# Kernel tuning notes

Hardware: AMD Instinct MI355X
Metric: run time of the kernel (lower is better)

The kernel has to match this reference:

```python
import jax, jax.numpy as jnp
import numpy as np
from jax.scipy.special import logsumexp

B, S, H, T = 64, 512, 768, 9

def setup_inputs() -> dict:
    key = jax.random.key(0)
    ks = jax.random.split(key, 6)
    return {
        "encoder_out": jax.random.normal(ks[0], (B, S, H), jnp.float32),
        "labels": jax.random.randint(ks[1], (B, S), 0, T, jnp.int32),
        "mask": jnp.ones((B, S), jnp.int32),
        "lengths": jnp.full((B,), S, jnp.int32),
        "fc_w": jax.random.normal(ks[2], (T, H), jnp.float32) * 0.02,
        "fc_b": jnp.zeros((T,), jnp.float32),
        "start_trans": jax.random.uniform(ks[3], (T,), jnp.float32, -0.1, 0.1),
        "end_trans": jax.random.uniform(ks[4], (T,), jnp.float32, -0.1, 0.1),
        "trans": jax.random.uniform(ks[5], (T, T), jnp.float32, -0.1, 0.1),
    }

def crf_log_likelihood(em, tg, mk, start, end, trans):
    # em: [S,B,T], tg: [S,B], mk: [S,B] float. torchcrf forward (reduction='none').
    barange = jnp.arange(em.shape[1])
    # --- numerator: score of the gold path ---
    score0 = start[tg[0]] + em[0][barange, tg[0]]
    def num_step(carry, x):
        score, prev = carry
        em_i, tg_i, mk_i = x
        score = score + (trans[prev, tg_i] + em_i[barange, tg_i]) * mk_i
        prev = jnp.where(mk_i > 0, tg_i, prev)
        return (score, prev), None
    (score, prev), _ = jax.lax.scan(num_step, (score0, tg[0]), (em[1:], tg[1:], mk[1:]))
    numerator = score + end[prev]
    # --- denominator: log partition via forward algorithm ---
    alpha = start[None, :] + em[0]  # [B,T]
    def den_step(alpha, x):
        em_i, mk_i = x
        nxt = logsumexp(alpha[:, :, None] + trans[None] + em_i[:, None, :], axis=1)
        return jnp.where(mk_i[:, None] > 0, nxt, alpha), None
    alpha, _ = jax.lax.scan(den_step, alpha, (em[1:], mk[1:]))
    denominator = logsumexp(alpha + end[None, :], axis=1)
    return numerator - denominator  # [B]

def crf_viterbi(em, mk, start, end, trans):
    # em: [S,B,T], mk: [S,B] float. Returns best path [S,B].
    barange = jnp.arange(em.shape[1])
    alpha = start[None, :] + em[0]  # [B,T]
    idT = jnp.arange(em.shape[2])[None, :]
    def fwd_step(alpha, x):
        em_i, mk_i = x
        scores = alpha[:, :, None] + trans[None]  # [B, T_prev, T_cur]
        bp = jnp.argmax(scores, axis=1)           # [B,T]
        nxt = jnp.max(scores, axis=1) + em_i
        valid = mk_i[:, None] > 0
        return jnp.where(valid, nxt, alpha), jnp.where(valid, bp, idT)
    alpha, bps = jax.lax.scan(fwd_step, alpha, (em[1:], mk[1:]))  # bps: [S-1,B,T]
    last = jnp.argmax(alpha + end[None, :], axis=1)  # [B]
    def back_step(tag, bp):
        prev = bp[barange, tag]
        return prev, prev
    _, path_head = jax.lax.scan(back_step, last, bps, reverse=True)  # [S-1,B]
    return jnp.concatenate([path_head, last[None, :]], axis=0)  # [S,B]

def reference(encoder_out, labels, mask, lengths, fc_w, fc_b, start_trans, end_trans, trans):
    # dropout in eval mode == identity
    emissions = jnp.einsum('bsh,th->bst', encoder_out, fc_w) + fc_b  # [B,S,T]
    em = jnp.swapaxes(emissions, 0, 1)               # [S,B,T]
    tg = jnp.swapaxes(labels, 0, 1)                  # [S,B]
    mk = jnp.swapaxes(mask, 0, 1).astype(emissions.dtype)
    ll = crf_log_likelihood(em, tg, mk, start_trans, end_trans, trans)  # [B]
    ner_loss = jnp.mean(-ll)
    path = crf_viterbi(em, mk, start_trans, end_trans, trans)  # [S,B]
    ner_predict = jnp.swapaxes(path, 0, 1)  # [B,S]
    return ner_loss, ner_predict, lengths
```

## Files before the change

kernel.cpp:

```cpp
#include <hip/hip_runtime.h>

#define Bsz 64
#define Ssz 512
#define Hsz 768
#define Tsz 9
#define NCH 16
#define LOG2E 1.4426950408889634f
#define LN2F  0.6931471805599453f
#define PSTR 17

__device__ __forceinline__ int SK(int s) { return s * Tsz + ((s >> 5) << 1); }

__global__ __launch_bounds__(256, 1) void emis_kernel(
    const float* __restrict__ x, const float* __restrict__ fcw,
    const float* __restrict__ fcb, float* __restrict__ em,
    int* __restrict__ cnt) {
    __shared__ __align__(16) float4 w4[Tsz * Hsz / 4];
    __shared__ float bias[Tsz];
    __shared__ float part[16 * Tsz * PSTR];
    const int tid = threadIdx.x;
    if (blockIdx.x == 0 && tid == 0) *cnt = 0;
    const float4* fw4 = reinterpret_cast<const float4*>(fcw);
#pragma unroll
    for (int i = 0; i < 7; ++i) {
        const int o = tid + i * 256;
        if (o < 1728) w4[o] = fw4[o];
    }
    if (tid < Tsz) bias[tid] = fcb[tid];
    __syncthreads();

    const int p = tid >> 4, l = tid & 15;
    const size_t pos0 = (size_t)blockIdx.x * 32;
    const float4* xr0 = reinterpret_cast<const float4*>(x + (pos0 + p) * Hsz);
    const float4* xr1 = reinterpret_cast<const float4*>(x + (pos0 + 16 + p) * Hsz);

    float acc[Tsz][2];
#pragma unroll
    for (int t = 0; t < Tsz; ++t) { acc[t][0] = 0.0f; acc[t][1] = 0.0f; }

#pragma unroll 4
    for (int i = 0; i < 12; ++i) {
        const float4 xv0 = xr0[i * 16 + l];
        const float4 xv1 = xr1[i * 16 + l];
#pragma unroll
        for (int t = 0; t < Tsz; ++t) {
            const float4 wv = w4[t * 192 + i * 16 + l];
            acc[t][0] = fmaf(xv0.x, wv.x, fmaf(xv0.y, wv.y,
                        fmaf(xv0.z, wv.z, fmaf(xv0.w, wv.w, acc[t][0]))));
            acc[t][1] = fmaf(xv1.x, wv.x, fmaf(xv1.y, wv.y,
                        fmaf(xv1.z, wv.z, fmaf(xv1.w, wv.w, acc[t][1]))));
        }
    }

#pragma unroll
    for (int k = 0; k < 2; ++k) {
        __syncthreads();
#pragma unroll
        for (int t = 0; t < Tsz; ++t) part[(p * Tsz + t) * PSTR + l] = acc[t][k];
        __syncthreads();
        if (tid < 16 * Tsz) {
            const int pq = tid / Tsz, t = tid - pq * Tsz;
            float s = bias[t];
#pragma unroll
            for (int l2 = 0; l2 < 16; ++l2) s += part[(pq * Tsz + t) * PSTR + l2];
            em[(pos0 + (size_t)k * 16 + pq) * Tsz + t] = s;
        }
    }
}

__global__ __launch_bounds__(256, 1) void scan_kernel(
    const float* __restrict__ em, const int* __restrict__ mask,
    const float* __restrict__ trans, float* __restrict__ R2,
    float* __restrict__ MV) {
    __shared__ float Tlds[81];
    __shared__ float Elds[81];
    const int tid = threadIdx.x;
    if (tid < 81) {
        const float t = trans[tid];
        Tlds[tid] = t;
        Elds[tid] = exp2f(t * LOG2E);
    }
    __syncthreads();

    const int wid = tid >> 6, ln = tid & 63;
    const int q = ln / 9;
    const int j = ln - q * 9;
    const int W = blockIdx.x * 4 + wid;
    const int rho = W * 7 + q;
    if (q >= 7 || rho >= 2048 * Tsz) return;

    const int a = rho % Tsz;
    const int bc2 = rho / Tsz;
    const bool isLSE = bc2 < 1024;
    const int bc = isLSE ? bc2 : bc2 - 1024;
    const int b = bc >> 4, c = bc & 15;
    const int lb = 9 * q;

    const float* emb = em + (size_t)b * Ssz * Tsz;
    const int* mkb = mask + b * Ssz;
    const int s_lo = c * 32 + 1;
    const int s_hi = min(c * 32 + 32, Ssz - 1);

    float ec = emb[s_lo * Tsz + j];
    int mc = mkb[s_lo];

    if (isLSE) {
        float Ecol[Tsz];
#pragma unroll
        for (int i = 0; i < Tsz; ++i) Ecol[i] = Elds[i * Tsz + j];
        float pp = (j == a) ? 1.0f : 0.0f;
        float K = 0.0f;
        for (int s = s_lo; s <= s_hi; ++s) {
            const int sp = (s < s_hi) ? s + 1 : s;
            const float en = emb[sp * Tsz + j];
            const int mn = mkb[sp];
            float g = __shfl(pp, lb, 64) * Ecol[0];
#pragma unroll
            for (int i = 1; i < Tsz; ++i)
                g = fmaf(__shfl(pp, lb + i, 64), Ecol[i], g);
            const float np = g * exp2f(ec * LOG2E);
            if (mc > 0) pp = np;
            if (((s - s_lo) & 7) == 7) {
                float ss = __shfl(pp, lb, 64);
#pragma unroll
                for (int i = 1; i < Tsz; ++i) ss += __shfl(pp, lb + i, 64);
                K += __log2f(ss);
                const float inv = 1.0f / ss;
                pp *= inv;
            }
            ec = en; mc = mn;
        }
        R2[((size_t)bc * Tsz + a) * Tsz + j] = K + __log2f(pp);
    } else {
        float Tcol[Tsz];
#pragma unroll
        for (int i = 0; i < Tsz; ++i) Tcol[i] = Tlds[i * Tsz + j];
        float pp = (j == a) ? 0.0f : -1e30f;
        for (int s = s_lo; s <= s_hi; ++s) {
            const int sp = (s < s_hi) ? s + 1 : s;
            const float en = emb[sp * Tsz + j];
            const int mn = mkb[sp];
            float g = __shfl(pp, lb, 64) + Tcol[0];
#pragma unroll
            for (int i = 1; i < Tsz; ++i)
                g = fmaxf(g, __shfl(pp, lb + i, 64) + Tcol[i]);
            if (mc > 0) pp = g + ec;
            ec = en; mc = mn;
        }
        MV[(size_t)bc * 81 + a * Tsz + j] = pp;
    }
}

__device__ __forceinline__ void amax9(const float (&v)[Tsz], float& bv, int& bi) {
    float w01v = (v[1] > v[0]) ? v[1] : v[0]; int w01i = (v[1] > v[0]) ? 1 : 0;
    float w23v = (v[3] > v[2]) ? v[3] : v[2]; int w23i = (v[3] > v[2]) ? 3 : 2;
    float w45v = (v[5] > v[4]) ? v[5] : v[4]; int w45i = (v[5] > v[4]) ? 5 : 4;
    float w67v = (v[7] > v[6]) ? v[7] : v[6]; int w67i = (v[7] > v[6]) ? 7 : 6;
    float x03v = (w23v > w01v) ? w23v : w01v; int x03i = (w23v > w01v) ? w23i : w01i;
    float x47v = (w67v > w45v) ? w67v : w45v; int x47i = (w67v > w45v) ? w67i : w45i;
    float y07v = (x47v > x03v) ? x47v : x03v; int y07i = (x47v > x03v) ? x47i : x03i;
    bv = (v[8] > y07v) ? v[8] : y07v;
    bi = (v[8] > y07v) ? 8 : y07i;
}

__global__ __launch_bounds__(192, 1) void vit3_kernel(
    const float* __restrict__ em, const int* __restrict__ labels,
    const int* __restrict__ mask, const int* __restrict__ lengths,
    const float* __restrict__ start_t, const float* __restrict__ end_t,
    const float* __restrict__ trans, const float* __restrict__ R2,
    const float* __restrict__ MV, float* __restrict__ out_path,
    float* __restrict__ ll, float* __restrict__ dout, int* __restrict__ cnt) {
    __shared__ __align__(16) float em_s[4640];
    __shared__ __align__(16) int   mk_s[Ssz];
    __shared__ __align__(16) float mv_s[NCH * 81];
    __shared__ __align__(16) float r2_s[NCH * 81];
    __shared__ float tr_s[81];
    __shared__ float st_s[12], en_s[12];
    __shared__ __align__(16) float alc[2][NCH][12];
    __shared__ float a2c[2][12];
    __shared__ unsigned char bp[(Ssz - 1) * Tsz];
    __shared__ unsigned char mapA[64][12], mapB[64][12];
    __shared__ float den_sh, num_sh;
    __shared__ int lastf;

    const int b = blockIdx.x, tid = threadIdx.x;
    const int wv = tid >> 6, ln = tid & 63;
    const int c = tid / 12, j9 = tid % 12;
    const float* emb = em + (size_t)b * Ssz * Tsz;
    const int* mkb = mask + b * Ssz;
    const int* lbb = labels + b * Ssz;

    for (int i = tid; i < Ssz * Tsz; i += 192) {
        const int s = i / 9, j = i - s * 9;
        em_s[SK(s) + j] = emb[i];
    }
    for (int i = tid; i < Ssz; i += 192) mk_s[i] = mkb[i];
    {
        const float4* v4 = reinterpret_cast<const float4*>(MV + (size_t)b * NCH * 81);
        float4* vd = reinterpret_cast<float4*>(mv_s);
        for (int i = tid; i < NCH * 81 / 4; i += 192) vd[i] = v4[i];
        const float4* r4 = reinterpret_cast<const float4*>(R2 + (size_t)b * NCH * 81);
        float4* rd = reinterpret_cast<float4*>(r2_s);
        for (int i = tid; i < NCH * 81 / 4; i += 192) rd[i] = r4[i];
        if (tid < 81) tr_s[tid] = trans[tid];
        if (tid >= 96 && tid < 96 + Tsz) {
            st_s[tid - 96] = start_t[tid - 96];
            en_s[tid - 96] = end_t[tid - 96];
        }
    }
    __syncthreads();

    float tc[Tsz];
    const int jj = (j9 < Tsz) ? j9 : Tsz - 1;
#pragma unroll
    for (int i = 0; i < Tsz; ++i) tc[i] = tr_s[i * Tsz + jj];

    float aj = 0.0f;
    if (c == 0 && j9 < Tsz) {
        aj = st_s[j9] + em_s[j9];
        alc[0][0][j9] = aj;
    }
    if (wv == 1 && ln < Tsz) a2c[0][ln] = (st_s[ln] + em_s[ln]) * LOG2E;

    for (int r = 0; r < NCH; ++r) {
        __syncthreads();
        if (r < NCH - 1 && c == r + 1 && j9 < Tsz) {
            const float* M = &mv_s[r * 81];
            float m = alc[0][r][0] + M[j9];
#pragma unroll
            for (int i = 1; i < Tsz; ++i)
                m = fmaxf(m, alc[0][r][i] + M[i * Tsz + j9]);
            aj = m;
            alc[0][c][j9] = m;
        }
        if (wv == 1 && ln < Tsz) {
            const float* Rr = &r2_s[r * 81];
            float xi[Tsz];
#pragma unroll
            for (int i = 0; i < Tsz; ++i) xi[i] = a2c[r & 1][i] + Rr[i * Tsz + ln];
            float m = xi[0];
#pragma unroll
            for (int i = 1; i < Tsz; ++i) m = fmaxf(m, xi[i]);
            float sm = 0.0f;
#pragma unroll
            for (int i = 0; i < Tsz; ++i) sm += exp2f(xi[i] - m);
            a2c[(r + 1) & 1][ln] = m + __log2f(sm);
        }
    }

    int pb = 0;
    for (int k = 0; k < 32; ++k) {
        __syncthreads();
        const int s = c * 32 + 1 + k;
        if (j9 < Tsz && s <= Ssz - 1) {
            const int mk = mk_s[s];
            float av[12];
            const float4* ap = reinterpret_cast<const float4*>(&alc[pb][c][0]);
            *reinterpret_cast<float4*>(&av[0]) = ap[0];
            *reinterpret_cast<float4*>(&av[4]) = ap[1];
            *reinterpret_cast<float4*>(&av[8]) = ap[2];
            float v[Tsz];
#pragma unroll
            for (int i = 0; i < Tsz; ++i) v[i] = av[i] + tc[i];
            float bv; int bi;
            amax9(v, bv, bi);
            bp[(s - 1) * Tsz + j9] = (unsigned char)((mk > 0) ? bi : j9);
            if (mk > 0) aj = bv + em_s[SK(s) + j9];
        }
        if (j9 < Tsz) alc[1 - pb][c][j9] = aj;
        pb ^= 1;
    }
    __syncthreads();

    float bb = alc[0][NCH - 1][0] + en_s[0];
    int last = 0;
#pragma unroll
    for (int q = 1; q < Tsz; ++q) {
        const float qq = alc[0][NCH - 1][q] + en_s[q];
        if (qq > bb) { bb = qq; last = q; }
    }

    const int lo = ln * 8;
    const int hi = min(lo + 7, Ssz - 2);
    if (wv == 0) {
        int xf[Tsz];
#pragma unroll
        for (int t = 0; t < Tsz; ++t) xf[t] = t;
        for (int k = hi; k >= lo; --k) {
#pragma unroll
            for (int t = 0; t < Tsz; ++t) xf[t] = bp[k * Tsz + xf[t]];
        }
#pragma unroll
        for (int t = 0; t < Tsz; ++t) mapA[ln][t] = (unsigned char)xf[t];
    } else if (wv == 1) {
        if (ln == 0) {
            float xv[Tsz];
#pragma unroll
            for (int i = 0; i < Tsz; ++i) xv[i] = a2c[0][i] + en_s[i] * LOG2E;
            float m = xv[0];
#pragma unroll
            for (int i = 1; i < Tsz; ++i) m = fmaxf(m, xv[i]);
            float sm = 0.0f;
#pragma unroll
            for (int i = 0; i < Tsz; ++i) sm += exp2f(xv[i] - m);
            den_sh = m + __log2f(sm);
        }
    } else {
        float part = 0.0f;
        for (int s = 1 + ln; s < Ssz; s += 64) {
            if (mk_s[s] > 0) {
                const int tg = lbb[s];
                int pq = s - 1;
                while (pq > 0 && mk_s[pq] == 0) --pq;
                part += tr_s[lbb[pq] * Tsz + tg] + em_s[SK(s) + tg];
            }
        }
#pragma unroll
        for (int off = 32; off >= 1; off >>= 1) part += __shfl_xor(part, off, 64);
        if (ln == 0) {
            const int tg0 = lbb[0];
            float num = part + st_s[tg0] + em_s[tg0];
            int pq = Ssz - 1;
            while (pq > 0 && mk_s[pq] == 0) --pq;
            num += en_s[lbb[pq]];
            num_sh = num;
        }
    }

#define VIT_RND(CUR, NXT, D)                                               \
    {                                                                      \
        unsigned char nn[Tsz];                                             \
        if (wv == 0) {                                                     \
            const int o = ln + (D);                                        \
            if (o < 64) {                                                  \
                _Pragma("unroll") for (int t = 0; t < Tsz; ++t)            \
                    nn[t] = CUR[ln][CUR[o][t]];                            \
            } else {                                                       \
                _Pragma("unroll") for (int t = 0; t < Tsz; ++t)            \
                    nn[t] = CUR[ln][t];                                    \
            }                                                              \
        }                                                                  \
        __syncthreads();                                                   \
        if (wv == 0) {                                                     \
            _Pragma("unroll") for (int t = 0; t < Tsz; ++t)                \
                NXT[ln][t] = nn[t];                                        \
        }                                                                  \
        __syncthreads();                                                   \
    }
    VIT_RND(mapA, mapB, 1)
    VIT_RND(mapB, mapA, 2)
    VIT_RND(mapA, mapB, 4)
    VIT_RND(mapB, mapA, 8)
    VIT_RND(mapA, mapB, 16)
    VIT_RND(mapB, mapA, 32)
#undef VIT_RND

    if (wv == 0) {
        int t = (ln == 63) ? last : (int)mapA[ln + 1][last];
        float* op = out_path + (size_t)b * Ssz;
        for (int k = hi; k >= lo; --k) {
            t = bp[k * Tsz + t];
            op[k] = (float)t;
        }
        if (ln == 0) op[Ssz - 1] = (float)last;
    }
    if (b == 0 && wv == 2) dout[1 + Bsz * Ssz + ln] = (float)lengths[ln];

    if (tid == 0) {
        ll[b] = num_sh - den_sh * LN2F;
        __threadfence();
        lastf = (atomicAdd(cnt, 1) == Bsz - 1) ? 1 : 0;
    }
    __syncthreads();
    if (lastf && wv == 0) {
        __threadfence();
        float v = ll[ln];
#pragma unroll
        for (int off = 32; off >= 1; off >>= 1) v += __shfl_xor(v, off, 64);
        if (ln == 0) dout[0] = -v * (1.0f / (float)Bsz);
    }
}

extern "C" void kernel_launch(void* const* d_in, const int* in_sizes, int n_in,
                              void* d_out, int out_size, void* d_ws, size_t ws_size,
                              hipStream_t stream) {
    const float* enc    = (const float*)d_in[0];
    const int*   labels = (const int*)d_in[1];
    const int*   mask   = (const int*)d_in[2];
    const int*   lengths= (const int*)d_in[3];
    const float* fcw    = (const float*)d_in[4];
    const float* fcb    = (const float*)d_in[5];
    const float* startt = (const float*)d_in[6];
    const float* endt   = (const float*)d_in[7];
    const float* trans  = (const float*)d_in[8];

    float* out = (float*)d_out;
    float* em  = (float*)d_ws;
    float* R2  = em + (size_t)Bsz * Ssz * Tsz;
    float* MV  = R2 + (size_t)Bsz * NCH * 81;
    float* ll  = MV + (size_t)Bsz * NCH * 81;
    int*   cnt = (int*)(ll + Bsz);

    emis_kernel<<<Bsz * Ssz / 32, 256, 0, stream>>>(enc, fcw, fcb, em, cnt);
    const int row_tasks = 2 * Bsz * NCH * Tsz;
    scan_kernel<<<(row_tasks + 27) / 28, 256, 0, stream>>>(em, mask, trans, R2, MV);
    vit3_kernel<<<Bsz, 192, 0, stream>>>(em, labels, mask, lengths, startt, endt,
                                         trans, R2, MV, out + 1, ll, out, cnt);
}
```

Measured before the change: 65.87 us.

## Fuse emission projection with per-chunk CRF scan into a single kernel

Merges the emission GEMV kernel and the chunked forward/Viterbi scan kernel into one kernel, one block per 32-step chunk. Each block keeps its emissions and mask in shared memory and recomputes the first emission row of the next chunk, so the scan no longer reads em back from global memory and one launch is removed. The cost is some redundant projection work per block and only 18 of 256 threads running the serial scan, which leaves most of the block idle during that phase.

Measured after the change: 71.03 us. +7.8%, slower.

```diff
diff --git a/kernel.cpp b/kernel.cpp
--- a/kernel.cpp
+++ b/kernel.cpp
@@ -11,15 +11,27 @@
 
 __device__ __forceinline__ int SK(int s) { return s * Tsz + ((s >> 5) << 1); }
 
-__global__ __launch_bounds__(256, 1) void emis_kernel(
+__global__ __launch_bounds__(256, 1) void emscan2_kernel(
     const float* __restrict__ x, const float* __restrict__ fcw,
-    const float* __restrict__ fcb, float* __restrict__ em,
-    int* __restrict__ cnt) {
+    const float* __restrict__ fcb, const int* __restrict__ mask,
+    const float* __restrict__ trans, float* __restrict__ em,
+    float* __restrict__ R2, float* __restrict__ MV, int* __restrict__ cnt) {
     __shared__ __align__(16) float4 w4[Tsz * Hsz / 4];
     __shared__ float bias[Tsz];
     __shared__ float part[16 * Tsz * PSTR];
+    __shared__ float em_w[33 * Tsz];
+    __shared__ int   mk_w[33];
+    __shared__ float Elds[81];
+    __shared__ float Tlds[81];
+
     const int tid = threadIdx.x;
-    if (blockIdx.x == 0 && tid == 0) *cnt = 0;
+    const int bc = blockIdx.x;
+    const int b = bc >> 4, c = bc & 15;
+    const int base = c * 32;
+    const size_t pos0 = (size_t)bc * 32;
+
+    if (bc == 0 && tid == 0) *cnt = 0;
+
     const float4* fw4 = reinterpret_cast<const float4*>(fcw);
 #pragma unroll
     for (int i = 0; i < 7; ++i) {
@@ -27,100 +39,108 @@
         if (o < 1728) w4[o] = fw4[o];
     }
     if (tid < Tsz) bias[tid] = fcb[tid];
+    if (tid >= 16 && tid < 16 + 81) {
+        const float t = trans[tid - 16];
+        Tlds[tid - 16] = t;
+        Elds[tid - 16] = exp2f(t * LOG2E);
+    }
+    if (tid >= 128 && tid < 128 + 33) {
+        const int s = base + (tid - 128);
+        mk_w[tid - 128] = (s < Ssz) ? mask[b * Ssz + s] : 0;
+    }
     __syncthreads();
 
     const int p = tid >> 4, l = tid & 15;
-    const size_t pos0 = (size_t)blockIdx.x * 32;
-    const float4* xr0 = reinterpret_cast<const float4*>(x + (pos0 + p) * Hsz);
-    const float4* xr1 = reinterpret_cast<const float4*>(x + (pos0 + 16 + p) * Hsz);
-
-    float acc[Tsz][2];
-#pragma unroll
-    for (int t = 0; t < Tsz; ++t) { acc[t][0] = 0.0f; acc[t][1] = 0.0f; }
-
+    {
+        const float4* xr0 = reinterpret_cast<const float4*>(x + (pos0 + p) * Hsz);
+        const float4* xr1 = reinterpret_cast<const float4*>(x + (pos0 + 16 + p) * Hsz);
+        float acc[Tsz][2];
+#pragma unroll
+        for (int t = 0; t < Tsz; ++t) { acc[t][0] = 0.0f; acc[t][1] = 0.0f; }
 #pragma unroll 4
-    for (int i = 0; i < 12; ++i) {
-        const float4 xv0 = xr0[i * 16 + l];
-        const float4 xv1 = xr1[i * 16 + l];
-#pragma unroll
-        for (int t = 0; t < Tsz; ++t) {
-            const float4 wv = w4[t * 192 + i * 16 + l];
-            acc[t][0] = fmaf(xv0.x, wv.x, fmaf(xv0.y, wv.y,
-                        fmaf(xv0.z, wv.z, fmaf(xv0.w, wv.w, acc[t][0]))));
-            acc[t][1] = fmaf(xv1.x, wv.x, fmaf(xv1.y, wv.y,
-                        fmaf(xv1.z, wv.z, fmaf(xv1.w, wv.w, acc[t][1]))));
-        }
-    }
-
-#pragma unroll
-    for (int k = 0; k < 2; ++k) {
+        for (int i = 0; i < 12; ++i) {
+            const float4 xv0 = xr0[i * 16 + l];
+            const float4 xv1 = xr1[i * 16 + l];
+#pragma unroll
+            for (int t = 0; t < Tsz; ++t) {
+                const float4 wv = w4[t * 192 + i * 16 + l];
+                acc[t][0] = fmaf(xv0.x, wv.x, fmaf(xv0.y, wv.y,
+                            fmaf(xv0.z, wv.z, fmaf(xv0.w, wv.w, acc[t][0]))));
+                acc[t][1] = fmaf(xv1.x, wv.x, fmaf(xv1.y, wv.y,
+                            fmaf(xv1.z, wv.z, fmaf(xv1.w, wv.w, acc[t][1]))));
+            }
+        }
+#pragma unroll
+        for (int k = 0; k < 2; ++k) {
+            __syncthreads();
+#pragma unroll
+            for (int t = 0; t < Tsz; ++t) part[(p * Tsz + t) * PSTR + l] = acc[t][k];
+            __syncthreads();
+            if (tid < 16 * Tsz) {
+                const int pq = tid / Tsz, t = tid - pq * Tsz;
+                float s = bias[t];
+#pragma unroll
+                for (int l2 = 0; l2 < 16; ++l2) s += part[(pq * Tsz + t) * PSTR + l2];
+                em[(pos0 + (size_t)k * 16 + pq) * Tsz + t] = s;
+                em_w[(k * 16 + pq) * Tsz + t] = s;
+            }
+        }
+    }
+    if (c < 15) {
+        float acc2[Tsz];
+#pragma unroll
+        for (int t = 0; t < Tsz; ++t) acc2[t] = 0.0f;
+        if (tid < 16) {
+            const float4* xr2 = reinterpret_cast<const float4*>(x + (pos0 + 32) * Hsz);
+#pragma unroll 4
+            for (int i = 0; i < 12; ++i) {
+                const float4 xv = xr2[i * 16 + l];
+#pragma unroll
+                for (int t = 0; t < Tsz; ++t) {
+                    const float4 wv = w4[t * 192 + i * 16 + l];
+                    acc2[t] = fmaf(xv.x, wv.x, fmaf(xv.y, wv.y,
+                              fmaf(xv.z, wv.z, fmaf(xv.w, wv.w, acc2[t]))));
+                }
+            }
+        }
         __syncthreads();
-#pragma unroll
-        for (int t = 0; t < Tsz; ++t) part[(p * Tsz + t) * PSTR + l] = acc[t][k];
+        if (tid < 16) {
+#pragma unroll
+            for (int t = 0; t < Tsz; ++t) part[t * PSTR + l] = acc2[t];
+        }
         __syncthreads();
-        if (tid < 16 * Tsz) {
-            const int pq = tid / Tsz, t = tid - pq * Tsz;
-            float s = bias[t];
-#pragma unroll
-            for (int l2 = 0; l2 < 16; ++l2) s += part[(pq * Tsz + t) * PSTR + l2];
-            em[(pos0 + (size_t)k * 16 + pq) * Tsz + t] = s;
-        }
-    }
-}
-
-__global__ __launch_bounds__(256, 1) void scan_kernel(
-    const float* __restrict__ em, const int* __restrict__ mask,
-    const float* __restrict__ trans, float* __restrict__ R2,
-    float* __restrict__ MV) {
-    __shared__ float Tlds[81];
-    __shared__ float Elds[81];
-    const int tid = threadIdx.x;
-    if (tid < 81) {
-        const float t = trans[tid];
-        Tlds[tid] = t;
-        Elds[tid] = exp2f(t * LOG2E);
+        if (tid < Tsz) {
+            float s = bias[tid];
+#pragma unroll
+            for (int l2 = 0; l2 < 16; ++l2) s += part[tid * PSTR + l2];
+            em_w[32 * Tsz + tid] = s;
+        }
     }
     __syncthreads();
 
-    const int wid = tid >> 6, ln = tid & 63;
+    const int wv = tid >> 6, ln = tid & 63;
     const int q = ln / 9;
     const int j = ln - q * 9;
-    const int W = blockIdx.x * 4 + wid;
-    const int rho = W * 7 + q;
-    if (q >= 7 || rho >= 2048 * Tsz) return;
-
-    const int a = rho % Tsz;
-    const int bc2 = rho / Tsz;
-    const bool isLSE = bc2 < 1024;
-    const int bc = isLSE ? bc2 : bc2 - 1024;
-    const int b = bc >> 4, c = bc & 15;
+    const int tsk = wv * 7 + q;
+    if (wv >= 3 || q >= 7 || tsk >= 18) return;
     const int lb = 9 * q;
-
-    const float* emb = em + (size_t)b * Ssz * Tsz;
-    const int* mkb = mask + b * Ssz;
-    const int s_lo = c * 32 + 1;
-    const int s_hi = min(c * 32 + 32, Ssz - 1);
-
-    float ec = emb[s_lo * Tsz + j];
-    int mc = mkb[s_lo];
-
-    if (isLSE) {
+    const int ns = (c == 15) ? 31 : 32;
+
+    if (tsk < 9) {
+        const int a = tsk;
         float Ecol[Tsz];
 #pragma unroll
         for (int i = 0; i < Tsz; ++i) Ecol[i] = Elds[i * Tsz + j];
         float pp = (j == a) ? 1.0f : 0.0f;
         float K = 0.0f;
-        for (int s = s_lo; s <= s_hi; ++s) {
-            const int sp = (s < s_hi) ? s + 1 : s;
-            const float en = emb[sp * Tsz + j];
-            const int mn = mkb[sp];
+        for (int r = 1; r <= ns; ++r) {
             float g = __shfl(pp, lb, 64) * Ecol[0];
 #pragma unroll
             for (int i = 1; i < Tsz; ++i)
                 g = fmaf(__shfl(pp, lb + i, 64), Ecol[i], g);
-            const float np = g * exp2f(ec * LOG2E);
-            if (mc > 0) pp = np;
-            if (((s - s_lo) & 7) == 7) {
+            const float np = g * exp2f(em_w[r * Tsz + j] * LOG2E);
+            if (mk_w[r] > 0) pp = np;
+            if (((r - 1) & 7) == 7) {
                 float ss = __shfl(pp, lb, 64);
 #pragma unroll
                 for (int i = 1; i < Tsz; ++i) ss += __shfl(pp, lb + i, 64);
@@ -128,24 +148,20 @@
                 const float inv = 1.0f / ss;
                 pp *= inv;
             }
-            ec = en; mc = mn;
         }
         R2[((size_t)bc * Tsz + a) * Tsz + j] = K + __log2f(pp);
     } else {
+        const int a = tsk - 9;
         float Tcol[Tsz];
 #pragma unroll
         for (int i = 0; i < Tsz; ++i) Tcol[i] = Tlds[i * Tsz + j];
         float pp = (j == a) ? 0.0f : -1e30f;
-        for (int s = s_lo; s <= s_hi; ++s) {
-            const int sp = (s < s_hi) ? s + 1 : s;
-            const float en = emb[sp * Tsz + j];
-            const int mn = mkb[sp];
+        for (int r = 1; r <= ns; ++r) {
             float g = __shfl(pp, lb, 64) + Tcol[0];
 #pragma unroll
             for (int i = 1; i < Tsz; ++i)
                 g = fmaxf(g, __shfl(pp, lb + i, 64) + Tcol[i]);
-            if (mc > 0) pp = g + ec;
-            ec = en; mc = mn;
+            if (mk_w[r] > 0) pp = g + em_w[r * Tsz + j];
         }
         MV[(size_t)bc * 81 + a * Tsz + j] = pp;
     }
@@ -401,9 +417,8 @@
     float* ll  = MV + (size_t)Bsz * NCH * 81;
     int*   cnt = (int*)(ll + Bsz);
 
-    emis_kernel<<<Bsz * Ssz / 32, 256, 0, stream>>>(enc, fcw, fcb, em, cnt);
-    const int row_tasks = 2 * Bsz * NCH * Tsz;
-    scan_kernel<<<(row_tasks + 27) / 28, 256, 0, stream>>>(em, mask, trans, R2, MV);
+    emscan2_kernel<<<Bsz * NCH, 256, 0, stream>>>(enc, fcw, fcb, mask, trans,
+                                                  em, R2, MV, cnt);
     vit3_kernel<<<Bsz, 192, 0, stream>>>(em, labels, mask, lengths, startt, endt,
                                          trans, R2, MV, out + 1, ll, out, cnt);
 }
```
